# Performance work log

Measured on AMD Instinct MI355X. Metric: run time of the kernel, lower is better.

Reference implementation:

```python
import jax, jax.numpy as jnp
import numpy as np
import math

D_MODEL = 768
N_HEADS = 12
D_HEAD = D_MODEL // N_HEADS


def setup_inputs() -> dict:
    key = jax.random.key(0)
    ks = jax.random.split(key, 5)
    x = jax.random.normal(ks[0], (2, 4096, D_MODEL), dtype=jnp.float32)
    s = 1.0 / math.sqrt(D_MODEL)
    W_qkv = jax.random.normal(ks[1], (D_MODEL, 3 * D_MODEL), dtype=jnp.float32) * s
    b_qkv = jnp.zeros((3 * D_MODEL,), dtype=jnp.float32)
    W_out = jax.random.normal(ks[2], (D_MODEL, D_MODEL), dtype=jnp.float32) * s
    b_out = jnp.zeros((D_MODEL,), dtype=jnp.float32)
    return {"x": x, "W_qkv": W_qkv, "b_qkv": b_qkv, "W_out": W_out, "b_out": b_out}


def reference(x, W_qkv, b_qkv, W_out, b_out):
    B, T, C = x.shape
    H, Dh = N_HEADS, D_HEAD
    qkv = x @ W_qkv + b_qkv                      # [B,T,3C]
    q, k, v = jnp.split(qkv, 3, axis=-1)
    q = q.reshape(B, T, H, Dh).transpose(0, 2, 1, 3)  # [B,H,T,Dh]
    k = k.reshape(B, T, H, Dh).transpose(0, 2, 1, 3)
    v = v.reshape(B, T, H, Dh).transpose(0, 2, 1, 3)
    att = jnp.einsum('bhqd,bhkd->bhqk', q, k) * (1.0 / math.sqrt(Dh))
    causal = jnp.tril(jnp.ones((T, T), dtype=bool))
    att = jnp.where(causal, att, -jnp.inf)
    att = jax.nn.softmax(att, axis=-1)
    out = jnp.einsum('bhqk,bhkd->bhqd', att, v)  # [B,H,T,Dh]
    out = out.transpose(0, 2, 1, 3).reshape(B, T, C)
    return out @ W_out + b_out
```

## Files before the change

### kernel.cpp

```cpp
#include <hip/hip_runtime.h>
#include <hip/hip_bf16.h>
#include <cstdint>

#define NH 12
#define DH 64
#define TSEQ 4096
#define BATCH 2
#define CDIM 768
#define MROWS (BATCH*TSEQ)

typedef __bf16 bf16x8 __attribute__((ext_vector_type(8)));
typedef __bf16 bf16x4 __attribute__((ext_vector_type(4)));
typedef bf16x8 bf16x8_a __attribute__((may_alias));
typedef bf16x4 bf16x4_a __attribute__((may_alias));
typedef float f32x4 __attribute__((ext_vector_type(4)));

__device__ __forceinline__ uint16_t f2bu(float f) {
  uint32_t u = __float_as_uint(f);
  u += 0x7fffu + ((u >> 16) & 1u);
  return (uint16_t)(u >> 16);
}

__device__ __forceinline__ float bu2f(uint16_t x) {
  return __uint_as_float(((uint32_t)x) << 16);
}

__device__ __forceinline__ void gload_lds16(const void* g, void* l) {
  __builtin_amdgcn_global_load_lds(
      (const __attribute__((address_space(1))) void*)g,
      (__attribute__((address_space(3))) void*)l, 16, 0, 0);
}

__global__ void cast_f32_bf16(const float* __restrict__ in, uint16_t* __restrict__ out, int n4) {
  int i = blockIdx.x * blockDim.x + threadIdx.x;
  int stride = gridDim.x * blockDim.x;
  for (; i < n4; i += stride) {
    float4 v = ((const float4*)in)[i];
    ushort4 o;
    o.x = f2bu(v.x); o.y = f2bu(v.y); o.z = f2bu(v.z); o.w = f2bu(v.w);
    ((ushort4*)out)[i] = o;
  }
}

__global__ void transpose_cast(const float* __restrict__ w, uint16_t* __restrict__ wt, int K, int N) {
  __shared__ float tile[32][33];
  int kb = blockIdx.x * 32, nb = blockIdx.y * 32;
  int tx = threadIdx.x & 31, ty = threadIdx.x >> 5;
  #pragma unroll
  for (int r = ty; r < 32; r += 8) tile[r][tx] = w[(size_t)(kb + r) * N + nb + tx];
  __syncthreads();
  #pragma unroll
  for (int r = ty; r < 32; r += 8) wt[(size_t)(nb + r) * K + kb + tx] = f2bu(tile[tx][r]);
}

__global__ __launch_bounds__(256) void gemm_qkv(
    const uint16_t* __restrict__ A, const uint16_t* __restrict__ Bt,
    const float* __restrict__ bias,
    uint16_t* __restrict__ q, uint16_t* __restrict__ k, uint16_t* __restrict__ v,
    int N, int K) {
  __shared__ uint16_t As[128 * 32];
  __shared__ uint16_t Bs[128 * 32];
  int tid = threadIdx.x;
  int w = tid >> 6, l = tid & 63;
  int lg = l >> 4, lr = l & 15;
  int mb = blockIdx.x * 128, nb = blockIdx.y * 128;
  int wr = (w >> 1) * 64, wc = (w & 1) * 64;
  f32x4 acc[4][4] = {};
  int srow = tid >> 2, scol = (tid & 3) * 8;
  const uint16_t* Ag = A + (size_t)(mb + srow) * K + scol;
  const uint16_t* Bg = Bt + (size_t)(nb + srow) * K + scol;
  char* AsB = (char*)As + (size_t)w * 1024;
  char* BsB = (char*)Bs + (size_t)w * 1024;
  size_t rowskip = (size_t)64 * K;
  for (int kb = 0; kb < K; kb += 32) {
    __syncthreads();
    gload_lds16(Ag + kb, AsB);
    gload_lds16(Ag + kb + rowskip, AsB + 4096);
    gload_lds16(Bg + kb, BsB);
    gload_lds16(Bg + kb + rowskip, BsB + 4096);
    __syncthreads();
    bf16x8 af[4], bfr[4];
    #pragma unroll
    for (int i = 0; i < 4; ++i)
      af[i] = *(const bf16x8_a*)(const void*)(As + (wr + i * 16 + lr) * 32 + lg * 8);
    #pragma unroll
    for (int i = 0; i < 4; ++i)
      bfr[i] = *(const bf16x8_a*)(const void*)(Bs + (wc + i * 16 + lr) * 32 + lg * 8);
    #pragma unroll
    for (int mi = 0; mi < 4; ++mi)
      #pragma unroll
      for (int ni = 0; ni < 4; ++ni)
        acc[mi][ni] = __builtin_amdgcn_mfma_f32_16x16x32_bf16(af[mi], bfr[ni], acc[mi][ni], 0, 0, 0);
  }
  #pragma unroll
  for (int mi = 0; mi < 4; ++mi) {
    #pragma unroll
    for (int ni = 0; ni < 4; ++ni) {
      int gm0 = mb + wr + mi * 16 + lg * 4;
      int gn = nb + wc + ni * 16 + lr;
      int which = gn / CDIM;
      int cc = gn - which * CDIM;
      int hh = cc >> 6, d = cc & 63;
      float bs = bias[gn];
      if (which == 2) {
        int b0 = gm0 >> 12, t0 = gm0 & 4095;
        ushort4 pk;
        pk.x = f2bu(acc[mi][ni][0] + bs);
        pk.y = f2bu(acc[mi][ni][1] + bs);
        pk.z = f2bu(acc[mi][ni][2] + bs);
        pk.w = f2bu(acc[mi][ni][3] + bs);
        *(ushort4*)&v[(((size_t)(b0 * NH + hh)) * DH + d) * TSEQ + t0] = pk;
      } else {
        uint16_t* dst = which ? k : q;
        float sc = which ? 1.0f : 0.1803368801111204f;
        #pragma unroll
        for (int j = 0; j < 4; ++j) {
          int gm = gm0 + j;
          int bb = gm >> 12, t = gm & 4095;
          float val = (acc[mi][ni][j] + bs) * sc;
          dst[(((size_t)(bb * NH + hh)) * TSEQ + t) * DH + d] = f2bu(val);
        }
      }
    }
  }
}

__global__ __launch_bounds__(256) void gemm_out(
    const uint16_t* __restrict__ A, const uint16_t* __restrict__ Bt,
    const float* __restrict__ bias, float* __restrict__ outf, int N, int K) {
  __shared__ uint16_t As[128 * 32];
  __shared__ uint16_t Bs[64 * 32];
  int tid = threadIdx.x;
  int w = tid >> 6, l = tid & 63;
  int lg = l >> 4, lr = l & 15;
  int mb = blockIdx.x * 128, nb = blockIdx.y * 64;
  int wr = w * 32;
  f32x4 acc[2][4] = {};
  int srow = tid >> 2, scol = (tid & 3) * 8;
  const uint16_t* Ag = A + (size_t)(mb + srow) * K + scol;
  const uint16_t* Bg = Bt + (size_t)(nb + srow) * K + scol;
  char* AsB = (char*)As + (size_t)w * 1024;
  char* BsB = (char*)Bs + (size_t)w * 1024;
  size_t rowskip = (size_t)64 * K;
  for (int kb = 0; kb < K; kb += 32) {
    __syncthreads();
    gload_lds16(Ag + kb, AsB);
    gload_lds16(Ag + kb + rowskip, AsB + 4096);
    gload_lds16(Bg + kb, BsB);
    __syncthreads();
    bf16x8 af[2], bfr[4];
    #pragma unroll
    for (int i = 0; i < 2; ++i)
      af[i] = *(const bf16x8_a*)(const void*)(As + (wr + i * 16 + lr) * 32 + lg * 8);
    #pragma unroll
    for (int i = 0; i < 4; ++i)
      bfr[i] = *(const bf16x8_a*)(const void*)(Bs + (i * 16 + lr) * 32 + lg * 8);
    #pragma unroll
    for (int mi = 0; mi < 2; ++mi)
      #pragma unroll
      for (int ni = 0; ni < 4; ++ni)
        acc[mi][ni] = __builtin_amdgcn_mfma_f32_16x16x32_bf16(af[mi], bfr[ni], acc[mi][ni], 0, 0, 0);
  }
  #pragma unroll
  for (int mi = 0; mi < 2; ++mi) {
    #pragma unroll
    for (int ni = 0; ni < 4; ++ni) {
      #pragma unroll
      for (int j = 0; j < 4; ++j) {
        int gm = mb + wr + mi * 16 + lg * 4 + j;
        int gn = nb + ni * 16 + lr;
        outf[(size_t)gm * N + gn] = acc[mi][ni][j] + bias[gn];
      }
    }
  }
}

__device__ __forceinline__ int lbase_qt(int qt) {
  return (qt < 22) ? (qt - 11) * 2 : 22 + (qt - 22) * 3;
}
__device__ __forceinline__ int ebase_qt(int qt) {
  return (qt < 22) ? (qt - 11) : 11 + (qt - 22) * 2;
}

__global__ __launch_bounds__(256) void attn_part(
    const uint16_t* __restrict__ Q, const uint16_t* __restrict__ K,
    const uint16_t* __restrict__ Vt, uint16_t* __restrict__ O,
    uint16_t* __restrict__ Pbuf, float* __restrict__ Pl) {
  int gid = blockIdx.x;
  int widx = gid / 24, bh = gid - widx * 24;
  int qt, c, nch;
  if (widx < 30) { qt = 31 - widx / 3; c = widx % 3; nch = 3; }
  else if (widx < 52) { int u = widx - 30; qt = 21 - (u >> 1); c = u & 1; nch = 2; }
  else { qt = 62 - widx; c = 0; nch = 1; }
  int ntile = 2 * qt + 2;
  int L = (ntile + nch - 1) / nch;
  int t0 = c * L;
  int t1 = min(ntile - 1, t0 + L - 1);

  int b = bh / NH, hd = bh - b * NH;
  size_t base = (size_t)bh * TSEQ * DH;
  int tid = threadIdx.x, w = tid >> 6, lane = tid & 63;
  int lg = lane >> 4, lr = lane & 15;
  __shared__ __align__(16) uint16_t Ks[64 * 64];
  __shared__ __align__(16) uint16_t Vs[64 * 64];
  __shared__ uint16_t Ps[4][16 * 64];
  char* pw = (char*)Ps[w];
  int srow = tid >> 3;
  int schunk = (tid & 7) ^ (srow & 7);
  const uint16_t* Kg0 = K + base + (size_t)srow * DH + schunk * 8;
  const uint16_t* Vg0 = Vt + base + (size_t)srow * TSEQ + schunk * 8;
  char* KsB = (char*)Ks + w * 1024;
  char* VsB = (char*)Vs + w * 1024;
  int swzA = (lg ^ (lr & 7)) << 4;
  int swzB = swzA ^ 64;

  int qb = qt * 128;
  int qgA = qb + w * 16 + lr;
  int qgB = qgA + 64;
  bf16x8 qA0 = *(const bf16x8_a*)(const void*)(Q + base + (size_t)qgA * DH + lg * 8);
  bf16x8 qA1 = *(const bf16x8_a*)(const void*)(Q + base + (size_t)qgA * DH + 32 + lg * 8);
  bf16x8 qB0 = *(const bf16x8_a*)(const void*)(Q + base + (size_t)qgB * DH + lg * 8);
  bf16x8 qB1 = *(const bf16x8_a*)(const void*)(Q + base + (size_t)qgB * DH + 32 + lg * 8);
  f32x4 oA[4] = {}, oB[4] = {};
  float lA = 0.f, lB = 0.f;
  int lg4 = lg * 4;
  int pofs = (lg & 1) * 8;

  for (int t = t0; t <= t1; ++t) {
    __syncthreads();
    {
      const uint16_t* kg_ = Kg0 + (size_t)t * (64 * DH);
      const uint16_t* vg_ = Vg0 + (size_t)t * 64;
      gload_lds16(kg_,           KsB);
      gload_lds16(kg_ + 32 * DH, KsB + 4096);
      gload_lds16(vg_,                     VsB);
      gload_lds16(vg_ + (size_t)32 * TSEQ, VsB + 4096);
    }
    __syncthreads();
    bool doA = (t <= 2 * qt);
    int kb0 = t * 64;
    f32x4 sA[4], sB[4];
    __builtin_amdgcn_s_setprio(1);
    #pragma unroll
    for (int ni = 0; ni < 4; ++ni) {
      const char* kbp = (const char*)Ks + (ni * 16 + lr) * 128;
      bf16x8 kf0 = *(const bf16x8_a*)(kbp + swzA);
      bf16x8 kf1 = *(const bf16x8_a*)(kbp + swzB);
      f32x4 s = {};
      s = __builtin_amdgcn_mfma_f32_16x16x32_bf16(kf0, qB0, s, 0, 0, 0);
      s = __builtin_amdgcn_mfma_f32_16x16x32_bf16(kf1, qB1, s, 0, 0, 0);
      sB[ni] = s;
      if (doA) {
        f32x4 sa = {};
        sa = __builtin_amdgcn_mfma_f32_16x16x32_bf16(kf0, qA0, sa, 0, 0, 0);
        sa = __builtin_amdgcn_mfma_f32_16x16x32_bf16(kf1, qA1, sa, 0, 0, 0);
        sA[ni] = sa;
      }
    }
    __builtin_amdgcn_s_setprio(0);
    bf16x8 pfA0, pfA1;
    if (doA) {
      if (t == 2 * qt) {
        int thr = qgA - kb0 - lg4;
        #pragma unroll
        for (int ni = 0; ni < 4; ++ni)
          #pragma unroll
          for (int j = 0; j < 4; ++j)
            sA[ni][j] = (16 * ni + j <= thr) ? sA[ni][j] : -1e30f;
      }
      #pragma unroll
      for (int ni = 0; ni < 4; ++ni) {
        float p0 = __builtin_amdgcn_exp2f(sA[ni][0]);
        float p1 = __builtin_amdgcn_exp2f(sA[ni][1]);
        float p2 = __builtin_amdgcn_exp2f(sA[ni][2]);
        float p3 = __builtin_amdgcn_exp2f(sA[ni][3]);
        lA += (p0 + p1) + (p2 + p3);
        bf16x4 pk;
        pk[0] = (__bf16)p0; pk[1] = (__bf16)p1; pk[2] = (__bf16)p2; pk[3] = (__bf16)p3;
        int chunkc = (2 * ni + (lg >> 1)) ^ (lr & 7);
        *(bf16x4_a*)(pw + lr * 128 + chunkc * 16 + pofs) = pk;
      }
      pfA0 = *(const bf16x8_a*)(pw + lr * 128 + swzA);
      pfA1 = *(const bf16x8_a*)(pw + lr * 128 + swzB);
    }
    {
      if (t == 2 * qt + 1) {
        int thr = qgB - kb0 - lg4;
        #pragma unroll
        for (int ni = 0; ni < 4; ++ni)
          #pragma unroll
          for (int j = 0; j < 4; ++j)
            sB[ni][j] = (16 * ni + j <= thr) ? sB[ni][j] : -1e30f;
      }
      #pragma unroll
      for (int ni = 0; ni < 4; ++ni) {
        float p0 = __builtin_amdgcn_exp2f(sB[ni][0]);
        float p1 = __builtin_amdgcn_exp2f(sB[ni][1]);
        float p2 = __builtin_amdgcn_exp2f(sB[ni][2]);
        float p3 = __builtin_amdgcn_exp2f(sB[ni][3]);
        lB += (p0 + p1) + (p2 + p3);
        bf16x4 pk;
        pk[0] = (__bf16)p0; pk[1] = (__bf16)p1; pk[2] = (__bf16)p2; pk[3] = (__bf16)p3;
        int chunkc = (2 * ni + (lg >> 1)) ^ (lr & 7);
        *(bf16x4_a*)(pw + lr * 128 + chunkc * 16 + pofs) = pk;
      }
    }
    bf16x8 pfB0 = *(const bf16x8_a*)(pw + lr * 128 + swzA);
    bf16x8 pfB1 = *(const bf16x8_a*)(pw + lr * 128 + swzB);
    __builtin_amdgcn_s_setprio(1);
    #pragma unroll
    for (int nd = 0; nd < 4; ++nd) {
      const char* vb = (const char*)Vs + (nd * 16 + lr) * 128;
      bf16x8 vf0 = *(const bf16x8_a*)(vb + swzA);
      bf16x8 vf1 = *(const bf16x8_a*)(vb + swzB);
      oB[nd] = __builtin_amdgcn_mfma_f32_16x16x32_bf16(pfB0, vf0, oB[nd], 0, 0, 0);
      oB[nd] = __builtin_amdgcn_mfma_f32_16x16x32_bf16(pfB1, vf1, oB[nd], 0, 0, 0);
      if (doA) {
        oA[nd] = __builtin_amdgcn_mfma_f32_16x16x32_bf16(pfA0, vf0, oA[nd], 0, 0, 0);
        oA[nd] = __builtin_amdgcn_mfma_f32_16x16x32_bf16(pfA1, vf1, oA[nd], 0, 0, 0);
      }
    }
    __builtin_amdgcn_s_setprio(0);
  }

  lA += __shfl_xor(lA, 16, 64); lA += __shfl_xor(lA, 32, 64);
  lB += __shfl_xor(lB, 16, 64); lB += __shfl_xor(lB, 32, 64);
  if (nch == 1) {
    float riA = 1.0f / lA, riB = 1.0f / lB;
    #pragma unroll
    for (int j = 0; j < 4; ++j) {
      float rvA = __shfl(riA, (lane & 48) | (lg4 + j), 64);
      float rvB = __shfl(riB, (lane & 48) | (lg4 + j), 64);
      int tA = qb + w * 16 + lg4 + j;
      size_t pA = (size_t)(b * TSEQ + tA) * CDIM + hd * DH + lr;
      size_t pB = pA + (size_t)64 * CDIM;
      #pragma unroll
      for (int nd = 0; nd < 4; ++nd) {
        O[pA + nd * 16] = f2bu(oA[nd][j] * rvA);
        O[pB + nd * 16] = f2bu(oB[nd][j] * rvB);
      }
    }
  } else {
    float* pl = Pl + (size_t)(bh * 64 + lbase_qt(qt) + c) * 128;
    if (lane < 16) {
      pl[w * 16 + lane] = lA;
      pl[64 + w * 16 + lane] = lB;
    }
    if (c == 0) {
      #pragma unroll
      for (int j = 0; j < 4; ++j) {
        int tA = qb + w * 16 + lg4 + j;
        size_t pA = (size_t)(b * TSEQ + tA) * CDIM + hd * DH + lr;
        size_t pB = pA + (size_t)64 * CDIM;
        #pragma unroll
        for (int nd = 0; nd < 4; ++nd) {
          O[pA + nd * 16] = f2bu(oA[nd][j]);
          O[pB + nd * 16] = f2bu(oB[nd][j]);
        }
      }
    } else {
      uint16_t* Pb = Pbuf + (size_t)(bh * 31 + ebase_qt(qt) + (c - 1)) * 8192;
      #pragma unroll
      for (int j = 0; j < 4; ++j) {
        int qlA = w * 16 + lg4 + j;
        #pragma unroll
        for (int nd = 0; nd < 4; ++nd) {
          Pb[qlA * 64 + nd * 16 + lr] = f2bu(oA[nd][j]);
          Pb[(64 + qlA) * 64 + nd * 16 + lr] = f2bu(oB[nd][j]);
        }
      }
    }
  }
}

__global__ __launch_bounds__(256) void attn_reduce(
    const uint16_t* __restrict__ Pbuf, const float* __restrict__ Pl,
    uint16_t* __restrict__ O) {
  int rid = blockIdx.x;
  int bh = rid / 21, qt = 11 + (rid - bh * 21);
  int nch = (qt >= 22) ? 3 : 2;
  int b = bh / NH, hd = bh - b * NH;
  int d = threadIdx.x & 63, qo = threadIdx.x >> 6;
  const float* pl = Pl + (size_t)(bh * 64 + lbase_qt(qt)) * 128;
  const uint16_t* pb = Pbuf + (size_t)(bh * 31 + ebase_qt(qt)) * 8192;
  #pragma unroll 4
  for (int q = qo; q < 128; q += 4) {
    float lsum = pl[q] + pl[128 + q];
    if (nch == 3) lsum += pl[256 + q];
    int t = qt * 128 + q;
    size_t po = (size_t)(b * TSEQ + t) * CDIM + hd * DH + d;
    float s = bu2f(O[po]) + bu2f(pb[q * 64 + d]);
    if (nch == 3) s += bu2f(pb[8192 + q * 64 + d]);
    O[po] = f2bu(s / lsum);
  }
}

extern "C" void kernel_launch(void* const* d_in, const int* in_sizes, int n_in,
                              void* d_out, int out_size, void* d_ws, size_t ws_size,
                              hipStream_t stream) {
  const float* x    = (const float*)d_in[0];
  const float* Wqkv = (const float*)d_in[1];
  const float* bqkv = (const float*)d_in[2];
  const float* Wout = (const float*)d_in[3];
  const float* bout = (const float*)d_in[4];
  float* out = (float*)d_out;
  char* ws = (char*)d_ws;

  uint16_t* Xb    = (uint16_t*)(ws + 0);
  uint16_t* Wqkvt = (uint16_t*)(ws + 12582912);
  uint16_t* Woutt = (uint16_t*)(ws + 16121856);
  uint16_t* Qb    = (uint16_t*)(ws + 17301504);
  uint16_t* Kb    = (uint16_t*)(ws + 29884416);
  uint16_t* Vtb   = (uint16_t*)(ws + 42467328);
  uint16_t* Ob    = (uint16_t*)(ws + 55050240);
  uint16_t* Pbuf  = Xb;
  float*    Pl    = (float*)Wqkvt;

  cast_f32_bf16<<<2048, 256, 0, stream>>>(x, Xb, (MROWS * CDIM) / 4);
  transpose_cast<<<dim3(24, 72), 256, 0, stream>>>(Wqkv, Wqkvt, 768, 2304);
  transpose_cast<<<dim3(24, 24), 256, 0, stream>>>(Wout, Woutt, 768, 768);
  gemm_qkv<<<dim3(64, 18), 256, 0, stream>>>(Xb, Wqkvt, bqkv, Qb, Kb, Vtb, 2304, 768);
  attn_part<<<1512, 256, 0, stream>>>(Qb, Kb, Vtb, Ob, Pbuf, Pl);
  attn_reduce<<<504, 256, 0, stream>>>(Pbuf, Pl, Ob);
  gemm_out<<<dim3(64, 12), 256, 0, stream>>>(Ob, Woutt, bout, out, 768, 768);
}
```

Baseline: 197.7 us.

## Double-buffer K/V tiles in attention and vectorize split-reduce kernel

```diff
diff --git a/kernel.cpp b/kernel.cpp
--- a/kernel.cpp
+++ b/kernel.cpp
@@ -201,16 +201,14 @@
   size_t base = (size_t)bh * TSEQ * DH;
   int tid = threadIdx.x, w = tid >> 6, lane = tid & 63;
   int lg = lane >> 4, lr = lane & 15;
-  __shared__ __align__(16) uint16_t Ks[64 * 64];
-  __shared__ __align__(16) uint16_t Vs[64 * 64];
+  __shared__ __align__(16) uint16_t Ks[2][64 * 64];
+  __shared__ __align__(16) uint16_t Vs[2][64 * 64];
   __shared__ uint16_t Ps[4][16 * 64];
   char* pw = (char*)Ps[w];
   int srow = tid >> 3;
   int schunk = (tid & 7) ^ (srow & 7);
   const uint16_t* Kg0 = K + base + (size_t)srow * DH + schunk * 8;
   const uint16_t* Vg0 = Vt + base + (size_t)srow * TSEQ + schunk * 8;
-  char* KsB = (char*)Ks + w * 1024;
-  char* VsB = (char*)Vs + w * 1024;
   int swzA = (lg ^ (lr & 7)) << 4;
   int swzB = swzA ^ 64;
 
@@ -226,24 +224,31 @@
   int lg4 = lg * 4;
   int pofs = (lg & 1) * 8;
 
+#define STAGE(bufi, tv) do { \
+    char* kd_ = (char*)Ks[bufi] + w * 1024; \
+    char* vd_ = (char*)Vs[bufi] + w * 1024; \
+    const uint16_t* kg_ = Kg0 + (size_t)(tv) * (64 * DH); \
+    const uint16_t* vg_ = Vg0 + (size_t)(tv) * 64; \
+    gload_lds16(kg_,           kd_); \
+    gload_lds16(kg_ + 32 * DH, kd_ + 4096); \
+    gload_lds16(vg_,                     vd_); \
+    gload_lds16(vg_ + (size_t)32 * TSEQ, vd_ + 4096); \
+  } while (0)
+
+  STAGE(0, t0);
+  __syncthreads();
+  int cur = 0;
   for (int t = t0; t <= t1; ++t) {
-    __syncthreads();
-    {
-      const uint16_t* kg_ = Kg0 + (size_t)t * (64 * DH);
-      const uint16_t* vg_ = Vg0 + (size_t)t * 64;
-      gload_lds16(kg_,           KsB);
-      gload_lds16(kg_ + 32 * DH, KsB + 4096);
-      gload_lds16(vg_,                     VsB);
-      gload_lds16(vg_ + (size_t)32 * TSEQ, VsB + 4096);
-    }
-    __syncthreads();
+    if (t + 1 <= t1) STAGE(cur ^ 1, t + 1);
+    const uint16_t* Kc = Ks[cur];
+    const uint16_t* Vc = Vs[cur];
     bool doA = (t <= 2 * qt);
     int kb0 = t * 64;
     f32x4 sA[4], sB[4];
     __builtin_amdgcn_s_setprio(1);
     #pragma unroll
     for (int ni = 0; ni < 4; ++ni) {
-      const char* kbp = (const char*)Ks + (ni * 16 + lr) * 128;
+      const char* kbp = (const char*)Kc + (ni * 16 + lr) * 128;
       bf16x8 kf0 = *(const bf16x8_a*)(kbp + swzA);
       bf16x8 kf1 = *(const bf16x8_a*)(kbp + swzB);
       f32x4 s = {};
@@ -310,7 +315,7 @@
     __builtin_amdgcn_s_setprio(1);
     #pragma unroll
     for (int nd = 0; nd < 4; ++nd) {
-      const char* vb = (const char*)Vs + (nd * 16 + lr) * 128;
+      const char* vb = (const char*)Vc + (nd * 16 + lr) * 128;
       bf16x8 vf0 = *(const bf16x8_a*)(vb + swzA);
       bf16x8 vf1 = *(const bf16x8_a*)(vb + swzB);
       oB[nd] = __builtin_amdgcn_mfma_f32_16x16x32_bf16(pfB0, vf0, oB[nd], 0, 0, 0);
@@ -321,7 +326,10 @@
       }
     }
     __builtin_amdgcn_s_setprio(0);
-  }
+    __syncthreads();
+    cur ^= 1;
+  }
+#undef STAGE
 
   lA += __shfl_xor(lA, 16, 64); lA += __shfl_xor(lA, 32, 64);
   lB += __shfl_xor(lB, 16, 64); lB += __shfl_xor(lB, 32, 64);
@@ -380,18 +388,32 @@
   int bh = rid / 21, qt = 11 + (rid - bh * 21);
   int nch = (qt >= 22) ? 3 : 2;
   int b = bh / NH, hd = bh - b * NH;
-  int d = threadIdx.x & 63, qo = threadIdx.x >> 6;
+  int tid = threadIdx.x;
   const float* pl = Pl + (size_t)(bh * 64 + lbase_qt(qt)) * 128;
   const uint16_t* pb = Pbuf + (size_t)(bh * 31 + ebase_qt(qt)) * 8192;
-  #pragma unroll 4
-  for (int q = qo; q < 128; q += 4) {
+  #pragma unroll
+  for (int it = 0; it < 8; ++it) {
+    int idx = it * 256 + tid;
+    int q = idx >> 4, dq = idx & 15;
     float lsum = pl[q] + pl[128 + q];
     if (nch == 3) lsum += pl[256 + q];
+    float linv = 1.0f / lsum;
     int t = qt * 128 + q;
-    size_t po = (size_t)(b * TSEQ + t) * CDIM + hd * DH + d;
-    float s = bu2f(O[po]) + bu2f(pb[q * 64 + d]);
-    if (nch == 3) s += bu2f(pb[8192 + q * 64 + d]);
-    O[po] = f2bu(s / lsum);
+    size_t po = (size_t)(b * TSEQ + t) * CDIM + hd * DH + dq * 4;
+    ushort4 ov = *(const ushort4*)&O[po];
+    ushort4 pv = *(const ushort4*)&pb[q * 64 + dq * 4];
+    float s0 = bu2f(ov.x) + bu2f(pv.x);
+    float s1 = bu2f(ov.y) + bu2f(pv.y);
+    float s2 = bu2f(ov.z) + bu2f(pv.z);
+    float s3 = bu2f(ov.w) + bu2f(pv.w);
+    if (nch == 3) {
+      ushort4 pv2 = *(const ushort4*)&pb[8192 + q * 64 + dq * 4];
+      s0 += bu2f(pv2.x); s1 += bu2f(pv2.y); s2 += bu2f(pv2.z); s3 += bu2f(pv2.w);
+    }
+    ushort4 o;
+    o.x = f2bu(s0 * linv); o.y = f2bu(s1 * linv);
+    o.z = f2bu(s2 * linv); o.w = f2bu(s3 * linv);
+    *(ushort4*)&O[po] = o;
   }
 }
 
```

Result: faster. 179.9 us (-9.0%).
